# Optimization experiments

Hardware: AMD Instinct MI355X
Metric: run time of the kernel (lower is better)

## Reference

```python
import jax, jax.numpy as jnp
import numpy as np
from jax.ops import segment_sum

N_PFAS, N_GW, N_SW = 50000, 200000, 20000
D_IN, D_OUT, D_EDGE = 32, 32, 3
E_PG, E_GP, E_PS, E_SP = 2000000, 2000000, 1000000, 1000000


def _params(key):
    ks = jax.random.split(key, 24)
    g = lambda k, s: jax.random.normal(k, s, dtype=jnp.float32) * 0.05
    p = {}
    # SAGEConvWithEdgeAttr for pg (pfas->gw) and gp (gw->pfas)
    for i, rel in enumerate(['pg', 'gp']):
        o = i * 5
        p[f'Wl_{rel}'] = g(ks[o + 0], (D_IN, D_OUT))
        p[f'bl_{rel}'] = g(ks[o + 1], (D_OUT,))
        p[f'Wr_{rel}'] = g(ks[o + 2], (D_IN, D_OUT))
        p[f'We_{rel}'] = g(ks[o + 3], (D_EDGE, D_OUT))
        p[f'be_{rel}'] = g(ks[o + 4], (D_OUT,))
    # plain SAGEConv for ps (pfas->sw) and sp (sw->pfas)
    for i, rel in enumerate(['ps', 'sp']):
        o = 10 + i * 3
        p[f'Wl_{rel}'] = g(ks[o + 0], (D_IN, D_OUT))
        p[f'bl_{rel}'] = g(ks[o + 1], (D_OUT,))
        p[f'Wr_{rel}'] = g(ks[o + 2], (D_IN, D_OUT))
    p['W_out'] = g(ks[16], (D_OUT, 1))
    p['b_out'] = g(ks[17], (1,))
    p['a_prelu'] = jnp.float32(0.25) * jnp.ones((1,), jnp.float32)
    return p


def setup_inputs() -> dict:
    key = jax.random.key(0)
    ks = jax.random.split(key, 16)
    inp = {
        'x_pfas': jax.random.normal(ks[0], (N_PFAS, D_IN), jnp.float32),
        'x_gw': jax.random.normal(ks[1], (N_GW, D_IN), jnp.float32),
        'x_sw': jax.random.normal(ks[2], (N_SW, D_IN), jnp.float32),
        'src_pg': jax.random.randint(ks[3], (E_PG,), 0, N_PFAS),
        'dst_pg': jax.random.randint(ks[4], (E_PG,), 0, N_GW),
        'ea_pg': jax.random.uniform(ks[5], (E_PG, D_EDGE), jnp.float32),
        'src_gp': jax.random.randint(ks[6], (E_GP,), 0, N_GW),
        'dst_gp': jax.random.randint(ks[7], (E_GP,), 0, N_PFAS),
        'ea_gp': jax.random.uniform(ks[8], (E_GP, D_EDGE), jnp.float32),
        'src_ps': jax.random.randint(ks[9], (E_PS,), 0, N_PFAS),
        'dst_ps': jax.random.randint(ks[10], (E_PS,), 0, N_SW),
        'src_sp': jax.random.randint(ks[11], (E_SP,), 0, N_SW),
        'dst_sp': jax.random.randint(ks[12], (E_SP,), 0, N_PFAS),
    }
    inp.update(_params(ks[13]))
    return inp


def _sage(x_src, x_dst, src, dst, Wl, bl, Wr, n_dst):
    # PyG SAGEConv: lin_l(mean_aggr(x_j)) + lin_r(x_dst); lin_r has no bias
    msg = x_src[src]                                   # [E, D_IN]
    s = segment_sum(msg, dst, num_segments=n_dst)      # [n_dst, D_IN]
    cnt = segment_sum(jnp.ones((src.shape[0],), x_src.dtype), dst, num_segments=n_dst)
    mean = s / jnp.maximum(cnt, 1.0)[:, None]
    return mean @ Wl + bl + x_dst @ Wr


def _edge_scatter_set(dst, ea_t, n_dst):
    # matches torch zeros.scatter_(0, col, edge_attr_transformed): overwrite at dst
    return jnp.zeros((n_dst, ea_t.shape[1]), ea_t.dtype).at[dst].set(ea_t)


def reference(x_pfas, x_gw, x_sw,
              src_pg, dst_pg, ea_pg,
              src_gp, dst_gp, ea_gp,
              src_ps, dst_ps, src_sp, dst_sp,
              Wl_pg, bl_pg, Wr_pg, We_pg, be_pg,
              Wl_gp, bl_gp, Wr_gp, We_gp, be_gp,
              Wl_ps, bl_ps, Wr_ps,
              Wl_sp, bl_sp, Wr_sp,
              W_out, b_out, a_prelu):
    # pfas -> gw (edge attrs)
    out_gw = _sage(x_pfas, x_gw, src_pg, dst_pg, Wl_pg, bl_pg, Wr_pg, N_GW)
    out_gw = out_gw + _edge_scatter_set(dst_pg, ea_pg @ We_pg + be_pg, N_GW)
    # gw -> pfas (edge attrs)
    out_pf1 = _sage(x_gw, x_pfas, src_gp, dst_gp, Wl_gp, bl_gp, Wr_gp, N_PFAS)
    out_pf1 = out_pf1 + _edge_scatter_set(dst_gp, ea_gp @ We_gp + be_gp, N_PFAS)
    # sw -> pfas (plain SAGE)
    out_pf2 = _sage(x_sw, x_pfas, src_sp, dst_sp, Wl_sp, bl_sp, Wr_sp, N_PFAS)
    # pfas -> sw (plain SAGE)
    out_sw = _sage(x_pfas, x_sw, src_ps, dst_ps, Wl_ps, bl_ps, Wr_ps, N_SW)
    # HeteroConv aggr='sum' over relations with same dst type, then relu
    h_pfas = jax.nn.relu(out_pf1 + out_pf2)
    h_gw = jax.nn.relu(out_gw)
    h_sw = jax.nn.relu(out_sw)
    # final linear + PReLU on gw_wells
    y = h_gw @ W_out + b_out                           # [N_GW, 1]
    y = jnp.where(y >= 0, y, a_prelu * y)
    return h_pfas, y, h_sw
```

## Files before the change

kernel.cpp:

```cpp
#include <hip/hip_runtime.h>
#include <hip/hip_fp16.h>

typedef unsigned int u32;

#define NPFAS 50000
#define NGW   200000
#define NSW   20000
#define D     32
#define EPG   2000000
#define EGP   2000000
#define EPS   1000000
#define ESP   1000000

#define NB_PG 782
#define NB_GP 782
#define NB_SP 391
#define NB_PS 313
#define CAP_PG 2880
#define CAP_GP 2880
#define CAP_SP 2880
#define CAP_PS 3584
#define SORT_MAX 3584
#define EIDM 0x1FFFFFu

#define ZGCUR    0
#define MAXE_PG  2304
#define MAXE_GP  202304
#define S_PG     252304
#define S_GP     6652304
#define S_SP     8252304
#define S_PS     9852304
#define CNT_PG   10492304
#define CNT_GP   10692304
#define CNT_SP   10742304
#define CNT_PS   10792304
#define REG_PG   10812304
#define REG_GP   13064464
#define REG_SP   15316624
#define REG_PS   16442704
#define XH_PFAS  17564496
#define XH_GW    18364496

__global__ __launch_bounds__(256) void convert_x(
    const float* __restrict__ xp, const float* __restrict__ xg, int* __restrict__ wsi)
{
    int i = blockIdx.x * 256 + threadIdx.x;
    __half2* hp = (__half2*)(wsi + XH_PFAS);
    __half2* hg = (__half2*)(wsi + XH_GW);
    const float2* fp = (const float2*)xp;
    const float2* fg = (const float2*)xg;
    if (i < NPFAS * D / 2) {
        float2 v = fp[i];
        hp[i] = __floats2half2_rn(v.x, v.y);
        return;
    }
    i -= NPFAS * D / 2;
    if (i < NGW * D / 2) {
        float2 v = fg[i];
        hg[i] = __floats2half2_rn(v.x, v.y);
    }
}

__device__ __forceinline__ void part4(
    const int* __restrict__ src, const int* __restrict__ dst,
    int e0, int e1, int nb, int cp, int cf, int pshift, int bbits, int roundSz,
    bool useEid,
    u32* __restrict__ region, int cap, int* __restrict__ gcur,
    u32* binData, u32* binCnt)
{
    u32 dlm = (1u << bbits) - 1u;
    for (int b = threadIdx.x; b < nb; b += 256) binCnt[b] = 0;
    __syncthreads();
    for (int base = e0; base < e1; base += roundSz) {
        int rend = base + roundSz; if (rend > e1) rend = e1;
        for (int e = base + (int)threadIdx.x; e < rend; e += 256) {
            int d = dst[e];
            int bk = d >> bbits;
            u32 payload = useEid ? (u32)e : (u32)src[e];
            u32 w0 = payload | (((u32)d & dlm) << pshift);
            u32 pos = atomicAdd(&binCnt[bk], 1u);
            if ((int)pos < cp) {
                binData[bk * cp + (int)pos] = w0;
            } else {
                int g = atomicAdd(&gcur[bk], 1);
                if (g < cap) region[(size_t)bk * cap + g] = w0;
            }
        }
        __syncthreads();
        bool last = (base + roundSz >= e1);
        for (int b = threadIdx.x; b < nb; b += 256) {
            int c = (int)binCnt[b];
            if (c > cp) c = cp;
            if (c >= cf || (last && c > 0)) {
                int g = atomicAdd(&gcur[b], c);
                int lim = cap - g; if (lim < 0) lim = 0; if (c > lim) c = lim;
                u32* dp = region + ((size_t)b * cap + g);
                for (int i = 0; i < c; i++) dp[i] = binData[b * cp + i];
                binCnt[b] = 0;
            }
        }
        __syncthreads();
    }
}

__global__ __launch_bounds__(256) void partition_all(
    const int* __restrict__ dst_pg,
    const int* __restrict__ dst_gp,
    const int* __restrict__ src_sp, const int* __restrict__ dst_sp,
    const int* __restrict__ src_ps, const int* __restrict__ dst_ps,
    int* __restrict__ wsi)
{
    __shared__ u32 binData[12512];
    __shared__ u32 binCnt[782];
    u32* ws = (u32*)wsi;
    int b = blockIdx.x;
    if (b < 160) {
        int e0 = b * (EPG / 160);
        part4(nullptr, dst_pg, e0, e0 + EPG / 160, NB_PG, 16, 10, 21, 8, 1024, true,
              ws + REG_PG, CAP_PG, wsi + ZGCUR + 0, binData, binCnt);
    } else if (b < 320) {
        int bb = b - 160;
        int e0 = bb * (EGP / 160);
        part4(nullptr, dst_gp, e0, e0 + EGP / 160, NB_GP, 16, 10, 21, 6, 1024, true,
              ws + REG_GP, CAP_GP, wsi + ZGCUR + 782, binData, binCnt);
    } else if (b < 416) {
        int bb = b - 320;
        int e0 = (int)(((long long)bb * ESP) / 96);
        int e1 = (int)(((long long)(bb + 1) * ESP) / 96);
        part4(src_sp, dst_sp, e0, e1, NB_SP, 32, 24, 15, 7, 1024, false,
              ws + REG_SP, CAP_SP, wsi + ZGCUR + 1564, binData, binCnt);
    } else {
        int bb = b - 416;
        int e0 = (int)(((long long)bb * EPS) / 96);
        int e1 = (int)(((long long)(bb + 1) * EPS) / 96);
        part4(src_ps, dst_ps, e0, e1, NB_PS, 32, 24, 16, 6, 1024, false,
              ws + REG_PS, CAP_PS, wsi + ZGCUR + 1955, binData, binCnt);
    }
}

__global__ __launch_bounds__(256) void sort_agg(
    const float* __restrict__ x_sw,
    const int* __restrict__ src_pg, const int* __restrict__ src_gp,
    int* __restrict__ wsi)
{
    __shared__ u32 sortedS[SORT_MAX];
    __shared__ int histS[256];
    __shared__ int startS[256];
    __shared__ int cursorS[256];
    __shared__ int mxS[256];
    __shared__ int wsum[4];

    float* wsf = (float*)wsi;
    u32* wsu = (u32*)wsi;
    int tid = threadIdx.x;
    int bid = blockIdx.x;

    const __half* xh = nullptr; const float* xf = nullptr;
    const u32* reg; const int* srcArr; int gi, cap, pshift, nbDst, dbase, ndst;
    u32 smask; bool useEid; float* sOut; float* cntOut; int* mxOut;

    if (bid < NB_PG) {
        xh = (const __half*)(wsi + XH_PFAS);
        reg = wsu + REG_PG + (size_t)bid * CAP_PG; gi = ZGCUR + bid;
        cap = CAP_PG; pshift = 21; smask = 0; useEid = true; srcArr = src_pg;
        nbDst = 256; dbase = bid << 8; ndst = NGW;
        sOut = wsf + S_PG; cntOut = wsf + CNT_PG; mxOut = wsi + MAXE_PG;
    } else if (bid < NB_PG + NB_GP) {
        int b = bid - NB_PG;
        xh = (const __half*)(wsi + XH_GW);
        reg = wsu + REG_GP + (size_t)b * CAP_GP; gi = ZGCUR + 782 + b;
        cap = CAP_GP; pshift = 21; smask = 0; useEid = true; srcArr = src_gp;
        nbDst = 64; dbase = b << 6; ndst = NPFAS;
        sOut = wsf + S_GP; cntOut = wsf + CNT_GP; mxOut = wsi + MAXE_GP;
    } else if (bid < NB_PG + NB_GP + NB_SP) {
        int b = bid - NB_PG - NB_GP;
        xf = x_sw;
        reg = wsu + REG_SP + (size_t)b * CAP_SP; gi = ZGCUR + 1564 + b;
        cap = CAP_SP; pshift = 15; smask = 0x7FFFu; useEid = false; srcArr = nullptr;
        nbDst = 128; dbase = b << 7; ndst = NPFAS;
        sOut = wsf + S_SP; cntOut = wsf + CNT_SP; mxOut = nullptr;
    } else {
        int b = bid - NB_PG - NB_GP - NB_SP;
        xh = (const __half*)(wsi + XH_PFAS);
        reg = wsu + REG_PS + (size_t)b * CAP_PS; gi = ZGCUR + 1955 + b;
        cap = CAP_PS; pshift = 16; smask = 0xFFFFu; useEid = false; srcArr = nullptr;
        nbDst = 64; dbase = b << 6; ndst = NSW;
        sOut = wsf + S_PS; cntOut = wsf + CNT_PS; mxOut = nullptr;
    }

    int nEnt = wsi[gi]; if (nEnt > cap) nEnt = cap;

    histS[tid] = 0;
    mxS[tid] = -1;
    __syncthreads();

    for (int i = tid; i < nEnt; i += 256) {
        u32 w0 = reg[i];
        int dl = (int)((w0 >> pshift) & 255u);
        atomicAdd(&histS[dl], 1);
        if (useEid) atomicMax(&mxS[dl], (int)(w0 & EIDM));
    }
    __syncthreads();

    {
        int v = histS[tid];
        int lane = tid & 63, w = tid >> 6;
        int incl = v;
#pragma unroll
        for (int off = 1; off < 64; off <<= 1) {
            int t = __shfl_up(incl, off);
            if (lane >= off) incl += t;
        }
        if (lane == 63) wsum[w] = incl;
        startS[tid] = incl - v;
    }
    __syncthreads();
    {
        int w = tid >> 6;
        int off = 0;
        for (int k = 0; k < w; k++) off += wsum[k];
        int st = startS[tid] + off;
        startS[tid] = st;
        cursorS[tid] = st;
    }
    __syncthreads();

    for (int i = tid; i < nEnt; i += 256) {
        u32 w0 = reg[i];
        int dl = (int)((w0 >> pshift) & 255u);
        int pos = atomicAdd(&cursorS[dl], 1);
        u32 sv = useEid ? (u32)srcArr[(int)(w0 & EIDM)] : (w0 & smask);
        if (pos < SORT_MAX) sortedS[pos] = sv;
    }
    __syncthreads();

    int wv = tid >> 6, lane = tid & 63, half = lane >> 5, f = lane & 31;
    for (int q = wv; q < nbDst; q += 4) {
        int dn = dbase + q;
        if (dn >= ndst) continue;
        int deg = histS[q];
        int p0 = startS[q];
        float a = 0.f;
        int i = half;
        if (xh) {
            for (; i + 6 < deg; i += 8) {
                int s0 = (int)sortedS[p0 + i];
                int s1 = (int)sortedS[p0 + i + 2];
                int s2 = (int)sortedS[p0 + i + 4];
                int s3 = (int)sortedS[p0 + i + 6];
                float v0 = __half2float(xh[(size_t)s0 * D + f]);
                float v1 = __half2float(xh[(size_t)s1 * D + f]);
                float v2 = __half2float(xh[(size_t)s2 * D + f]);
                float v3 = __half2float(xh[(size_t)s3 * D + f]);
                a += (v0 + v1) + (v2 + v3);
            }
            for (; i < deg; i += 2) a += __half2float(xh[(size_t)sortedS[p0 + i] * D + f]);
        } else {
            for (; i + 6 < deg; i += 8) {
                int s0 = (int)sortedS[p0 + i];
                int s1 = (int)sortedS[p0 + i + 2];
                int s2 = (int)sortedS[p0 + i + 4];
                int s3 = (int)sortedS[p0 + i + 6];
                float v0 = xf[(size_t)s0 * D + f];
                float v1 = xf[(size_t)s1 * D + f];
                float v2 = xf[(size_t)s2 * D + f];
                float v3 = xf[(size_t)s3 * D + f];
                a += (v0 + v1) + (v2 + v3);
            }
            for (; i < deg; i += 2) a += xf[(size_t)sortedS[p0 + i] * D + f];
        }
        a += __shfl_xor(a, 32);
        if (half == 0) sOut[(size_t)dn * D + f] = a;
        if (lane == 0) {
            cntOut[dn] = (float)deg;
            if (useEid) mxOut[dn] = mxS[q];
        }
    }
}

__global__ __launch_bounds__(256) void finalize_gw(
    const float* __restrict__ s, const float* __restrict__ cntF,
    const int* __restrict__ maxe,
    const float* __restrict__ x_gw,
    const float* __restrict__ ea,
    const float* __restrict__ Wl, const float* __restrict__ bl,
    const float* __restrict__ Wr, const float* __restrict__ We,
    const float* __restrict__ be,
    const float* __restrict__ W_out, const float* __restrict__ b_out,
    const float* __restrict__ a_prelu,
    float* __restrict__ y_out)
{
    __shared__ __align__(16) float WlT[D * D];
    __shared__ __align__(16) float WrT[D * D];
    __shared__ float WeT[3 * D];
    __shared__ float blS[D], beS[D], WoS[D];
    for (int i = threadIdx.x; i < D * D; i += blockDim.x) {
        int k = i / D, j = i % D;
        WlT[j * D + k] = Wl[i];
        WrT[j * D + k] = Wr[i];
    }
    for (int i = threadIdx.x; i < 3 * D; i += blockDim.x) {
        int k = i / D, j = i % D;
        WeT[j * 3 + k] = We[i];
    }
    if (threadIdx.x < D) {
        blS[threadIdx.x] = bl[threadIdx.x];
        beS[threadIdx.x] = be[threadIdx.x];
        WoS[threadIdx.x] = W_out[threadIdx.x];
    }
    __syncthreads();

    int n = blockIdx.x * blockDim.x + threadIdx.x;
    if (n >= NGW) return;

    float mean[D], xd[D];
    float inv = 1.0f / fmaxf(cntF[n], 1.0f);
    const float4* sp = (const float4*)(s + (size_t)n * D);
    const float4* xp = (const float4*)(x_gw + (size_t)n * D);
#pragma unroll
    for (int q = 0; q < D / 4; q++) {
        float4 sv = sp[q];
        mean[4*q+0] = sv.x * inv; mean[4*q+1] = sv.y * inv;
        mean[4*q+2] = sv.z * inv; mean[4*q+3] = sv.w * inv;
        float4 xv = xp[q];
        xd[4*q+0] = xv.x; xd[4*q+1] = xv.y; xd[4*q+2] = xv.z; xd[4*q+3] = xv.w;
    }
    int me = maxe[n];
    bool he = (me >= 0);
    float e0 = 0.f, e1 = 0.f, e2 = 0.f;
    if (he) {
        e0 = ea[(size_t)me * 3 + 0];
        e1 = ea[(size_t)me * 3 + 1];
        e2 = ea[(size_t)me * 3 + 2];
    }
    float yacc = 0.f;
    for (int j = 0; j < D; j++) {
        float o = blS[j] + (he ? beS[j] : 0.0f);
        const float4* wl4 = (const float4*)(WlT + j * D);
        const float4* wr4 = (const float4*)(WrT + j * D);
#pragma unroll
        for (int q = 0; q < D / 4; q++) {
            float4 wl = wl4[q], wr = wr4[q];
            o += mean[4*q+0]*wl.x + mean[4*q+1]*wl.y + mean[4*q+2]*wl.z + mean[4*q+3]*wl.w;
            o += xd[4*q+0]*wr.x + xd[4*q+1]*wr.y + xd[4*q+2]*wr.z + xd[4*q+3]*wr.w;
        }
        if (he) o += e0*WeT[j*3+0] + e1*WeT[j*3+1] + e2*WeT[j*3+2];
        float h = fmaxf(o, 0.0f);
        yacc += h * WoS[j];
    }
    float y = yacc + b_out[0];
    float ap = a_prelu[0];
    y_out[n] = (y >= 0.f) ? y : ap * y;
}

__global__ __launch_bounds__(256) void finalize_pfas(
    const float* __restrict__ s_gp, const float* __restrict__ cnt_gp,
    const int* __restrict__ maxe_gp,
    const float* __restrict__ s_sp, const float* __restrict__ cnt_sp,
    const float* __restrict__ x_pfas,
    const float* __restrict__ ea,
    const float* __restrict__ Wl_gp, const float* __restrict__ bl_gp,
    const float* __restrict__ Wr_gp, const float* __restrict__ We_gp,
    const float* __restrict__ be_gp,
    const float* __restrict__ Wl_sp, const float* __restrict__ bl_sp,
    const float* __restrict__ Wr_sp,
    float* __restrict__ h_out)
{
    __shared__ __align__(16) float WlgT[D * D];
    __shared__ __align__(16) float WlsT[D * D];
    __shared__ __align__(16) float WrcT[D * D];
    __shared__ float WeT[3 * D];
    __shared__ float blc[D], beS[D];
    for (int i = threadIdx.x; i < D * D; i += blockDim.x) {
        int k = i / D, j = i % D;
        WlgT[j * D + k] = Wl_gp[i];
        WlsT[j * D + k] = Wl_sp[i];
        WrcT[j * D + k] = Wr_gp[i] + Wr_sp[i];
    }
    for (int i = threadIdx.x; i < 3 * D; i += blockDim.x) {
        int k = i / D, j = i % D;
        WeT[j * 3 + k] = We_gp[i];
    }
    if (threadIdx.x < D) {
        blc[threadIdx.x] = bl_gp[threadIdx.x] + bl_sp[threadIdx.x];
        beS[threadIdx.x] = be_gp[threadIdx.x];
    }
    __syncthreads();

    int n = blockIdx.x * blockDim.x + threadIdx.x;
    if (n >= NPFAS) return;

    float mg[D], ms[D], xd[D];
    float invg = 1.0f / fmaxf(cnt_gp[n], 1.0f);
    float invs = 1.0f / fmaxf(cnt_sp[n], 1.0f);
    const float4* gp4 = (const float4*)(s_gp + (size_t)n * D);
    const float4* sp4 = (const float4*)(s_sp + (size_t)n * D);
    const float4* xp4 = (const float4*)(x_pfas + (size_t)n * D);
#pragma unroll
    for (int q = 0; q < D / 4; q++) {
        float4 a = gp4[q];
        mg[4*q+0] = a.x * invg; mg[4*q+1] = a.y * invg; mg[4*q+2] = a.z * invg; mg[4*q+3] = a.w * invg;
        float4 b = sp4[q];
        ms[4*q+0] = b.x * invs; ms[4*q+1] = b.y * invs; ms[4*q+2] = b.z * invs; ms[4*q+3] = b.w * invs;
        float4 c = xp4[q];
        xd[4*q+0] = c.x; xd[4*q+1] = c.y; xd[4*q+2] = c.z; xd[4*q+3] = c.w;
    }
    int me = maxe_gp[n];
    bool he = (me >= 0);
    float e0 = 0.f, e1 = 0.f, e2 = 0.f;
    if (he) {
        e0 = ea[(size_t)me * 3 + 0];
        e1 = ea[(size_t)me * 3 + 1];
        e2 = ea[(size_t)me * 3 + 2];
    }
    float* out = h_out + (size_t)n * D;
    for (int j = 0; j < D; j++) {
        float o = blc[j] + (he ? beS[j] : 0.0f);
        const float4* wg4 = (const float4*)(WlgT + j * D);
        const float4* ws4 = (const float4*)(WlsT + j * D);
        const float4* wc4 = (const float4*)(WrcT + j * D);
#pragma unroll
        for (int q = 0; q < D / 4; q++) {
            float4 wg = wg4[q], wsv = ws4[q], wc = wc4[q];
            o += mg[4*q+0]*wg.x + mg[4*q+1]*wg.y + mg[4*q+2]*wg.z + mg[4*q+3]*wg.w;
            o += ms[4*q+0]*wsv.x + ms[4*q+1]*wsv.y + ms[4*q+2]*wsv.z + ms[4*q+3]*wsv.w;
            o += xd[4*q+0]*wc.x + xd[4*q+1]*wc.y + xd[4*q+2]*wc.z + xd[4*q+3]*wc.w;
        }
        if (he) o += e0*WeT[j*3+0] + e1*WeT[j*3+1] + e2*WeT[j*3+2];
        out[j] = fmaxf(o, 0.0f);
    }
}

__global__ __launch_bounds__(256) void finalize_sw(
    const float* __restrict__ s, const float* __restrict__ cntF,
    const float* __restrict__ x_sw,
    const float* __restrict__ Wl, const float* __restrict__ bl,
    const float* __restrict__ Wr,
    float* __restrict__ h_out)
{
    __shared__ __align__(16) float WlT[D * D];
    __shared__ __align__(16) float WrT[D * D];
    __shared__ float blS[D];
    for (int i = threadIdx.x; i < D * D; i += blockDim.x) {
        int k = i / D, j = i % D;
        WlT[j * D + k] = Wl[i];
        WrT[j * D + k] = Wr[i];
    }
    if (threadIdx.x < D) blS[threadIdx.x] = bl[threadIdx.x];
    __syncthreads();

    int n = blockIdx.x * blockDim.x + threadIdx.x;
    if (n >= NSW) return;

    float mean[D], xd[D];
    float inv = 1.0f / fmaxf(cntF[n], 1.0f);
    const float4* sp = (const float4*)(s + (size_t)n * D);
    const float4* xp = (const float4*)(x_sw + (size_t)n * D);
#pragma unroll
    for (int q = 0; q < D / 4; q++) {
        float4 sv = sp[q];
        mean[4*q+0] = sv.x * inv; mean[4*q+1] = sv.y * inv;
        mean[4*q+2] = sv.z * inv; mean[4*q+3] = sv.w * inv;
        float4 xv = xp[q];
        xd[4*q+0] = xv.x; xd[4*q+1] = xv.y; xd[4*q+2] = xv.z; xd[4*q+3] = xv.w;
    }
    float* out = h_out + (size_t)n * D;
    for (int j = 0; j < D; j++) {
        float o = blS[j];
        const float4* wl4 = (const float4*)(WlT + j * D);
        const float4* wr4 = (const float4*)(WrT + j * D);
#pragma unroll
        for (int q = 0; q < D / 4; q++) {
            float4 wl = wl4[q], wr = wr4[q];
            o += mean[4*q+0]*wl.x + mean[4*q+1]*wl.y + mean[4*q+2]*wl.z + mean[4*q+3]*wl.w;
            o += xd[4*q+0]*wr.x + xd[4*q+1]*wr.y + xd[4*q+2]*wr.z + xd[4*q+3]*wr.w;
        }
        out[j] = fmaxf(o, 0.0f);
    }
}

extern "C" void kernel_launch(void* const* d_in, const int* in_sizes, int n_in,
                              void* d_out, int out_size, void* d_ws, size_t ws_size,
                              hipStream_t stream) {
    (void)in_sizes; (void)n_in; (void)out_size; (void)ws_size;
    const float* x_pfas = (const float*)d_in[0];
    const float* x_gw   = (const float*)d_in[1];
    const float* x_sw   = (const float*)d_in[2];
    const int*   src_pg = (const int*)d_in[3];
    const int*   dst_pg = (const int*)d_in[4];
    const float* ea_pg  = (const float*)d_in[5];
    const int*   src_gp = (const int*)d_in[6];
    const int*   dst_gp = (const int*)d_in[7];
    const float* ea_gp  = (const float*)d_in[8];
    const int*   src_ps = (const int*)d_in[9];
    const int*   dst_ps = (const int*)d_in[10];
    const int*   src_sp = (const int*)d_in[11];
    const int*   dst_sp = (const int*)d_in[12];
    const float* Wl_pg = (const float*)d_in[13];
    const float* bl_pg = (const float*)d_in[14];
    const float* Wr_pg = (const float*)d_in[15];
    const float* We_pg = (const float*)d_in[16];
    const float* be_pg = (const float*)d_in[17];
    const float* Wl_gp = (const float*)d_in[18];
    const float* bl_gp = (const float*)d_in[19];
    const float* Wr_gp = (const float*)d_in[20];
    const float* We_gp = (const float*)d_in[21];
    const float* be_gp = (const float*)d_in[22];
    const float* Wl_ps = (const float*)d_in[23];
    const float* bl_ps = (const float*)d_in[24];
    const float* Wr_ps = (const float*)d_in[25];
    const float* Wl_sp = (const float*)d_in[26];
    const float* bl_sp = (const float*)d_in[27];
    const float* Wr_sp = (const float*)d_in[28];
    const float* W_out = (const float*)d_in[29];
    const float* b_out = (const float*)d_in[30];
    const float* a_pre = (const float*)d_in[31];

    int*   wsi = (int*)d_ws;
    float* wsf = (float*)d_ws;

    hipMemsetAsync(wsi + ZGCUR, 0, 2304 * sizeof(int), stream);

    convert_x<<<(NPFAS * D / 2 + NGW * D / 2 + 255) / 256, 256, 0, stream>>>(
        x_pfas, x_gw, wsi);

    partition_all<<<512, 256, 0, stream>>>(dst_pg, dst_gp,
                                           src_sp, dst_sp, src_ps, dst_ps, wsi);

    sort_agg<<<NB_PG + NB_GP + NB_SP + NB_PS, 256, 0, stream>>>(
        x_sw, src_pg, src_gp, wsi);

    float* out    = (float*)d_out;
    float* h_pfas = out;
    float* y_out  = out + 1600000;
    float* h_sw   = out + 1800000;

    finalize_pfas<<<(NPFAS + 255) / 256, 256, 0, stream>>>(
        wsf + S_GP, wsf + CNT_GP, wsi + MAXE_GP, wsf + S_SP, wsf + CNT_SP,
        x_pfas, ea_gp,
        Wl_gp, bl_gp, Wr_gp, We_gp, be_gp,
        Wl_sp, bl_sp, Wr_sp, h_pfas);

    finalize_gw<<<(NGW + 255) / 256, 256, 0, stream>>>(
        wsf + S_PG, wsf + CNT_PG, wsi + MAXE_PG, x_gw, ea_pg,
        Wl_pg, bl_pg, Wr_pg, We_pg, be_pg,
        W_out, b_out, a_pre, y_out);

    finalize_sw<<<(NSW + 255) / 256, 256, 0, stream>>>(
        wsf + S_PS, wsf + CNT_PS, x_sw, Wl_ps, bl_ps, Wr_ps, h_sw);
}
```

Measured before the change: 493.7 us.

## Pack source index in partition and track max edge id with global atomics

The partition pass now reads src directly and packs the source node index into the binned word instead of the edge id. This removes the random gather of src_pg/src_gp by edge id in sort_agg. Max edge id per destination, needed for the scatter-set semantics, is now computed with global atomicMax during partitioning, using a new memset to -1. The trade is 4M global atomics and an extra memset against removing the shared-memory max tracking and the random index gathers.

```diff
diff --git a/kernel.cpp b/kernel.cpp
--- a/kernel.cpp
+++ b/kernel.cpp
@@ -21,7 +21,6 @@
 #define CAP_SP 2880
 #define CAP_PS 3584
 #define SORT_MAX 3584
-#define EIDM 0x1FFFFFu
 
 #define ZGCUR    0
 #define MAXE_PG  2304
@@ -64,7 +63,7 @@
 __device__ __forceinline__ void part4(
     const int* __restrict__ src, const int* __restrict__ dst,
     int e0, int e1, int nb, int cp, int cf, int pshift, int bbits, int roundSz,
-    bool useEid,
+    int* __restrict__ maxe,
     u32* __restrict__ region, int cap, int* __restrict__ gcur,
     u32* binData, u32* binCnt)
 {
@@ -76,8 +75,8 @@
         for (int e = base + (int)threadIdx.x; e < rend; e += 256) {
             int d = dst[e];
             int bk = d >> bbits;
-            u32 payload = useEid ? (u32)e : (u32)src[e];
-            u32 w0 = payload | (((u32)d & dlm) << pshift);
+            if (maxe) atomicMax(&maxe[d], e);
+            u32 w0 = (u32)src[e] | (((u32)d & dlm) << pshift);
             u32 pos = atomicAdd(&binCnt[bk], 1u);
             if ((int)pos < cp) {
                 binData[bk * cp + (int)pos] = w0;
@@ -104,8 +103,8 @@
 }
 
 __global__ __launch_bounds__(256) void partition_all(
-    const int* __restrict__ dst_pg,
-    const int* __restrict__ dst_gp,
+    const int* __restrict__ src_pg, const int* __restrict__ dst_pg,
+    const int* __restrict__ src_gp, const int* __restrict__ dst_gp,
     const int* __restrict__ src_sp, const int* __restrict__ dst_sp,
     const int* __restrict__ src_ps, const int* __restrict__ dst_ps,
     int* __restrict__ wsi)
@@ -116,38 +115,40 @@
     int b = blockIdx.x;
     if (b < 160) {
         int e0 = b * (EPG / 160);
-        part4(nullptr, dst_pg, e0, e0 + EPG / 160, NB_PG, 16, 10, 21, 8, 1024, true,
+        part4(src_pg, dst_pg, e0, e0 + EPG / 160, NB_PG, 16, 10, 21, 8, 1024,
+              wsi + MAXE_PG,
               ws + REG_PG, CAP_PG, wsi + ZGCUR + 0, binData, binCnt);
     } else if (b < 320) {
         int bb = b - 160;
         int e0 = bb * (EGP / 160);
-        part4(nullptr, dst_gp, e0, e0 + EGP / 160, NB_GP, 16, 10, 21, 6, 1024, true,
+        part4(src_gp, dst_gp, e0, e0 + EGP / 160, NB_GP, 16, 10, 21, 6, 1024,
+              wsi + MAXE_GP,
               ws + REG_GP, CAP_GP, wsi + ZGCUR + 782, binData, binCnt);
     } else if (b < 416) {
         int bb = b - 320;
         int e0 = (int)(((long long)bb * ESP) / 96);
         int e1 = (int)(((long long)(bb + 1) * ESP) / 96);
-        part4(src_sp, dst_sp, e0, e1, NB_SP, 32, 24, 15, 7, 1024, false,
+        part4(src_sp, dst_sp, e0, e1, NB_SP, 32, 24, 15, 7, 1024,
+              nullptr,
               ws + REG_SP, CAP_SP, wsi + ZGCUR + 1564, binData, binCnt);
     } else {
         int bb = b - 416;
         int e0 = (int)(((long long)bb * EPS) / 96);
         int e1 = (int)(((long long)(bb + 1) * EPS) / 96);
-        part4(src_ps, dst_ps, e0, e1, NB_PS, 32, 24, 16, 6, 1024, false,
+        part4(src_ps, dst_ps, e0, e1, NB_PS, 32, 24, 16, 6, 1024,
+              nullptr,
               ws + REG_PS, CAP_PS, wsi + ZGCUR + 1955, binData, binCnt);
     }
 }
 
 __global__ __launch_bounds__(256) void sort_agg(
     const float* __restrict__ x_sw,
-    const int* __restrict__ src_pg, const int* __restrict__ src_gp,
     int* __restrict__ wsi)
 {
     __shared__ u32 sortedS[SORT_MAX];
     __shared__ int histS[256];
     __shared__ int startS[256];
     __shared__ int cursorS[256];
-    __shared__ int mxS[256];
     __shared__ int wsum[4];
 
     float* wsf = (float*)wsi;
@@ -156,49 +157,47 @@
     int bid = blockIdx.x;
 
     const __half* xh = nullptr; const float* xf = nullptr;
-    const u32* reg; const int* srcArr; int gi, cap, pshift, nbDst, dbase, ndst;
-    u32 smask; bool useEid; float* sOut; float* cntOut; int* mxOut;
+    const u32* reg; int gi, cap, pshift, nbDst, dbase, ndst;
+    u32 smask; float* sOut; float* cntOut;
 
     if (bid < NB_PG) {
         xh = (const __half*)(wsi + XH_PFAS);
         reg = wsu + REG_PG + (size_t)bid * CAP_PG; gi = ZGCUR + bid;
-        cap = CAP_PG; pshift = 21; smask = 0; useEid = true; srcArr = src_pg;
+        cap = CAP_PG; pshift = 21; smask = 0x1FFFFFu;
         nbDst = 256; dbase = bid << 8; ndst = NGW;
-        sOut = wsf + S_PG; cntOut = wsf + CNT_PG; mxOut = wsi + MAXE_PG;
+        sOut = wsf + S_PG; cntOut = wsf + CNT_PG;
     } else if (bid < NB_PG + NB_GP) {
         int b = bid - NB_PG;
         xh = (const __half*)(wsi + XH_GW);
         reg = wsu + REG_GP + (size_t)b * CAP_GP; gi = ZGCUR + 782 + b;
-        cap = CAP_GP; pshift = 21; smask = 0; useEid = true; srcArr = src_gp;
+        cap = CAP_GP; pshift = 21; smask = 0x1FFFFFu;
         nbDst = 64; dbase = b << 6; ndst = NPFAS;
-        sOut = wsf + S_GP; cntOut = wsf + CNT_GP; mxOut = wsi + MAXE_GP;
+        sOut = wsf + S_GP; cntOut = wsf + CNT_GP;
     } else if (bid < NB_PG + NB_GP + NB_SP) {
         int b = bid - NB_PG - NB_GP;
         xf = x_sw;
         reg = wsu + REG_SP + (size_t)b * CAP_SP; gi = ZGCUR + 1564 + b;
-        cap = CAP_SP; pshift = 15; smask = 0x7FFFu; useEid = false; srcArr = nullptr;
+        cap = CAP_SP; pshift = 15; smask = 0x7FFFu;
         nbDst = 128; dbase = b << 7; ndst = NPFAS;
-        sOut = wsf + S_SP; cntOut = wsf + CNT_SP; mxOut = nullptr;
+        sOut = wsf + S_SP; cntOut = wsf + CNT_SP;
     } else {
         int b = bid - NB_PG - NB_GP - NB_SP;
         xh = (const __half*)(wsi + XH_PFAS);
         reg = wsu + REG_PS + (size_t)b * CAP_PS; gi = ZGCUR + 1955 + b;
-        cap = CAP_PS; pshift = 16; smask = 0xFFFFu; useEid = false; srcArr = nullptr;
+        cap = CAP_PS; pshift = 16; smask = 0xFFFFu;
         nbDst = 64; dbase = b << 6; ndst = NSW;
-        sOut = wsf + S_PS; cntOut = wsf + CNT_PS; mxOut = nullptr;
+        sOut = wsf + S_PS; cntOut = wsf + CNT_PS;
     }
 
     int nEnt = wsi[gi]; if (nEnt > cap) nEnt = cap;
 
     histS[tid] = 0;
-    mxS[tid] = -1;
     __syncthreads();
 
     for (int i = tid; i < nEnt; i += 256) {
         u32 w0 = reg[i];
         int dl = (int)((w0 >> pshift) & 255u);
         atomicAdd(&histS[dl], 1);
-        if (useEid) atomicMax(&mxS[dl], (int)(w0 & EIDM));
     }
     __syncthreads();
 
@@ -229,8 +228,7 @@
         u32 w0 = reg[i];
         int dl = (int)((w0 >> pshift) & 255u);
         int pos = atomicAdd(&cursorS[dl], 1);
-        u32 sv = useEid ? (u32)srcArr[(int)(w0 & EIDM)] : (w0 & smask);
-        if (pos < SORT_MAX) sortedS[pos] = sv;
+        if (pos < SORT_MAX) sortedS[pos] = w0 & smask;
     }
     __syncthreads();
 
@@ -271,10 +269,7 @@
         }
         a += __shfl_xor(a, 32);
         if (half == 0) sOut[(size_t)dn * D + f] = a;
-        if (lane == 0) {
-            cntOut[dn] = (float)deg;
-            if (useEid) mxOut[dn] = mxS[q];
-        }
+        if (lane == 0) cntOut[dn] = (float)deg;
     }
 }
 
@@ -520,15 +515,15 @@
     float* wsf = (float*)d_ws;
 
     hipMemsetAsync(wsi + ZGCUR, 0, 2304 * sizeof(int), stream);
+    hipMemsetAsync(wsi + MAXE_PG, 0xFF, 250000 * sizeof(int), stream);
 
     convert_x<<<(NPFAS * D / 2 + NGW * D / 2 + 255) / 256, 256, 0, stream>>>(
         x_pfas, x_gw, wsi);
 
-    partition_all<<<512, 256, 0, stream>>>(dst_pg, dst_gp,
+    partition_all<<<512, 256, 0, stream>>>(src_pg, dst_pg, src_gp, dst_gp,
                                            src_sp, dst_sp, src_ps, dst_ps, wsi);
 
-    sort_agg<<<NB_PG + NB_GP + NB_SP + NB_PS, 256, 0, stream>>>(
-        x_sw, src_pg, src_gp, wsi);
+    sort_agg<<<NB_PG + NB_GP + NB_SP + NB_PS, 256, 0, stream>>>(x_sw, wsi);
 
     float* out    = (float*)d_out;
     float* h_pfas = out;
```

New measurement: 592.0 us. +19.9%, slower.
